# Optimization experiments

Measured on AMD Instinct MI355X. Metric: run time of the kernel, lower is better.

The kernel has to match this reference:

```python
import jax, jax.numpy as jnp
import numpy as np

B, S, D, E, F = 4, 2048, 1024, 8, 4096


def setup_inputs() -> dict:
    key = jax.random.key(0)
    k0, k1, k2, k3 = jax.random.split(key, 4)
    x = jax.random.normal(k0, (B, S, D), dtype=jnp.float32)
    wg = jax.random.normal(k1, (D, E), dtype=jnp.float32) * 0.02       # router
    w_gate = jax.random.normal(k2, (E, D, F), dtype=jnp.float32) * 0.02  # expert gate_proj
    w_down = jax.random.normal(k3, (E, F, D), dtype=jnp.float32) * 0.02  # expert down_proj
    return {"x": x, "wg": wg, "w_gate": w_gate, "w_down": w_down}


def reference(x, wg, w_gate, w_down):
    Bb, Ss, Dd = x.shape
    Ee = wg.shape[1]
    T = Bb * Ss
    C = 2 * T // Ee  # GShard top-2 capacity
    tokens = x.reshape(T, Dd)

    # ---- Top2Gate (fp32 gating) ----
    logits = tokens.astype(jnp.float32) @ wg.astype(jnp.float32)  # [T,E]
    gates = jax.nn.softmax(logits, axis=-1)
    idx1 = jnp.argmax(gates, axis=-1)                              # [T]
    mask1 = jax.nn.one_hot(idx1, Ee, dtype=jnp.int32)
    logits_no1 = jnp.where(mask1 > 0, -jnp.inf, logits)
    idx2 = jnp.argmax(logits_no1, axis=-1)
    mask2 = jax.nn.one_hot(idx2, Ee, dtype=jnp.int32)

    g1 = jnp.take_along_axis(gates, idx1[:, None], axis=-1)[:, 0]
    g2 = jnp.take_along_axis(gates, idx2[:, None], axis=-1)[:, 0]
    denom = jnp.clip(g1 + g2, 1e-9, None)
    g1, g2 = g1 / denom, g2 / denom

    # slot positions: exclusive cumsum per expert; 2nd choice offset by expert's 1st-choice count
    loc1 = jnp.cumsum(mask1, axis=0) - mask1                       # [T,E]
    loc2 = jnp.cumsum(mask2, axis=0) - mask2 + jnp.sum(mask1, axis=0, keepdims=True)
    loc1_s = jnp.sum(loc1 * mask1, axis=-1)                        # [T]
    loc2_s = jnp.sum(loc2 * mask2, axis=-1)
    keep1 = (loc1_s < C).astype(x.dtype)
    keep2 = (loc2_s < C).astype(x.dtype)

    f1 = idx1 * C + jnp.minimum(loc1_s, C - 1)                     # flat [E*C] slot ids
    f2 = idx2 * C + jnp.minimum(loc2_s, C - 1)

    # ---- dispatch (scatter, equivalent to einsum with dispatch_mask) ----
    disp = jnp.zeros((Ee * C, Dd), dtype=x.dtype)
    disp = disp.at[f1].add(tokens * keep1[:, None])
    disp = disp.at[f2].add(tokens * keep2[:, None])
    disp = disp.reshape(Ee, C, Dd)

    # ---- per-expert FFN: down_proj(gelu(gate_proj(x))) ----
    h = jax.nn.gelu(jnp.einsum('ecd,edf->ecf', disp, w_gate), approximate=False)
    eo = jnp.einsum('ecf,efd->ecd', h, w_down).reshape(Ee * C, Dd)

    # ---- combine ----
    out = (g1 * keep1)[:, None].astype(x.dtype) * eo[f1] \
        + (g2 * keep2)[:, None].astype(x.dtype) * eo[f2]
    return out.reshape(Bb, Ss, Dd)
```

## Files before the change

kernel.cpp:

```cpp
#include <hip/hip_runtime.h>
#include <hip/hip_bf16.h>
#include <math.h>

#define TT 8192
#define DDIM 1024
#define EE 8
#define FF 4096
#define CCAP 2048
#define NSLOT 16384

typedef __attribute__((ext_vector_type(4))) float f32x4;
typedef __attribute__((ext_vector_type(8))) short bf16x8;

typedef const __attribute__((address_space(1))) void CGV;
typedef __attribute__((address_space(3))) void LDSV;

__device__ __forceinline__ short f2bf(float f) {
  unsigned u = __builtin_bit_cast(unsigned, f);
  u += 0x7fffu + ((u >> 16) & 1u);
  return (short)(u >> 16);
}
__device__ __forceinline__ float bf2f(short s) {
  unsigned u = ((unsigned)(unsigned short)s) << 16;
  return __builtin_bit_cast(float, u);
}

__global__ void __launch_bounds__(256) gate_kernel(const float* __restrict__ x,
    const float* __restrict__ wg, int* __restrict__ idx1, int* __restrict__ idx2,
    float* __restrict__ g1s, float* __restrict__ g2s) {
  int lane = threadIdx.x & 63;
  int t = blockIdx.x * 4 + (threadIdx.x >> 6);
  const float* xr = x + (size_t)t * DDIM;
  float acc[8];
#pragma unroll
  for (int e = 0; e < 8; ++e) acc[e] = 0.f;
#pragma unroll
  for (int i = 0; i < 4; ++i) {
    int d = lane * 4 + i * 256;
    f32x4 xv = *(const f32x4*)(xr + d);
#pragma unroll
    for (int j = 0; j < 4; ++j) {
      const f32x4* wr = (const f32x4*)(wg + (size_t)(d + j) * 8);
      f32x4 w0 = wr[0], w1 = wr[1];
#pragma unroll
      for (int e = 0; e < 4; ++e) { acc[e] += xv[j] * w0[e]; acc[e + 4] += xv[j] * w1[e]; }
    }
  }
#pragma unroll
  for (int e = 0; e < 8; ++e) {
#pragma unroll
    for (int o = 32; o > 0; o >>= 1) acc[e] += __shfl_xor(acc[e], o, 64);
  }
  if (lane == 0) {
    int i1 = 0; float l1 = acc[0];
#pragma unroll
    for (int e = 1; e < 8; ++e) if (acc[e] > l1) { l1 = acc[e]; i1 = e; }
    int i2 = -1; float l2 = -3.0e38f;
#pragma unroll
    for (int e = 0; e < 8; ++e) if (e != i1 && acc[e] > l2) { l2 = acc[e]; i2 = e; }
    float e2 = expf(l2 - l1);
    float inv = 1.f / (1.f + e2);
    idx1[t] = i1; idx2[t] = i2;
    g1s[t] = inv; g2s[t] = e2 * inv;
  }
}

__global__ void __launch_bounds__(1024) scan_kernel(const int* __restrict__ idx1,
    const int* __restrict__ idx2, const float* __restrict__ g1s, const float* __restrict__ g2s,
    int* __restrict__ f1, int* __restrict__ f2, float* __restrict__ gg1, float* __restrict__ gg2,
    int* __restrict__ slot_token) {
  __shared__ unsigned long long slo[1024], shi[1024];
  int tid = threadIdx.x;
  for (int i = tid; i < NSLOT; i += 1024) slot_token[i] = -1;
  int t0 = tid * 8;
  int e1[8], e2[8];
#pragma unroll
  for (int i = 0; i < 8; ++i) { e1[i] = idx1[t0 + i]; e2[i] = idx2[t0 + i]; }

  unsigned long long lo = 0, hi = 0;
#pragma unroll
  for (int i = 0; i < 8; ++i) {
    int e = e1[i];
    if (e < 4) lo += 1ull << (16 * e); else hi += 1ull << (16 * (e - 4));
  }
  slo[tid] = lo; shi[tid] = hi; __syncthreads();
  for (int off = 1; off < 1024; off <<= 1) {
    unsigned long long alo = 0, ahi = 0;
    if (tid >= off) { alo = slo[tid - off]; ahi = shi[tid - off]; }
    __syncthreads();
    slo[tid] += alo; shi[tid] += ahi;
    __syncthreads();
  }
  unsigned long long exlo = slo[tid] - lo, exhi = shi[tid] - hi;
  unsigned long long tlo = slo[1023], thi = shi[1023];
  __syncthreads();
  int base1[8], tot1[8];
#pragma unroll
  for (int e = 0; e < 4; ++e) {
    base1[e]     = (int)((exlo >> (16 * e)) & 0xFFFF);
    base1[e + 4] = (int)((exhi >> (16 * e)) & 0xFFFF);
    tot1[e]      = (int)((tlo  >> (16 * e)) & 0xFFFF);
    tot1[e + 4]  = (int)((thi  >> (16 * e)) & 0xFFFF);
  }

  lo = 0; hi = 0;
#pragma unroll
  for (int i = 0; i < 8; ++i) {
    int e = e2[i];
    if (e < 4) lo += 1ull << (16 * e); else hi += 1ull << (16 * (e - 4));
  }
  slo[tid] = lo; shi[tid] = hi; __syncthreads();
  for (int off = 1; off < 1024; off <<= 1) {
    unsigned long long alo = 0, ahi = 0;
    if (tid >= off) { alo = slo[tid - off]; ahi = shi[tid - off]; }
    __syncthreads();
    slo[tid] += alo; shi[tid] += ahi;
    __syncthreads();
  }
  exlo = slo[tid] - lo; exhi = shi[tid] - hi;
  int base2[8];
#pragma unroll
  for (int e = 0; e < 4; ++e) {
    base2[e]     = (int)((exlo >> (16 * e)) & 0xFFFF);
    base2[e + 4] = (int)((exhi >> (16 * e)) & 0xFFFF);
  }

#pragma unroll
  for (int i = 0; i < 8; ++i) {
    int t = t0 + i;
    int a = e1[i];
    int p1 = base1[a]++;
    int k1 = (p1 < CCAP);
    int s1 = a * CCAP + (k1 ? p1 : CCAP - 1);
    f1[t] = s1;
    gg1[t] = k1 ? g1s[t] : 0.f;
    if (k1) slot_token[s1] = t;

    int b = e2[i];
    int p2 = base2[b] + tot1[b];
    base2[b]++;
    int k2 = (p2 < CCAP);
    int s2 = b * CCAP + (k2 ? p2 : CCAP - 1);
    f2[t] = s2;
    gg2[t] = k2 ? g2s[t] : 0.f;
    if (k2) slot_token[s2] = t;
  }
}

__global__ void __launch_bounds__(128) dispatch_kernel(const float* __restrict__ x,
    const int* __restrict__ slot_token, short* __restrict__ disp) {
  int slot = blockIdx.x;
  int tid = threadIdx.x;
  int tok = slot_token[slot];
  short* dst = disp + (size_t)slot * DDIM + tid * 8;
  bf16x8 v;
  if (tok >= 0) {
    const float* src = x + (size_t)tok * DDIM + tid * 8;
    f32x4 a = *(const f32x4*)src;
    f32x4 b = *(const f32x4*)(src + 4);
#pragma unroll
    for (int j = 0; j < 4; ++j) { v[j] = f2bf(a[j]); v[j + 4] = f2bf(b[j]); }
  } else {
#pragma unroll
    for (int j = 0; j < 8; ++j) v[j] = 0;
  }
  *(bf16x8*)dst = v;
}

__global__ void __launch_bounds__(256) tconv_kernel(const float* __restrict__ in,
    short* __restrict__ outp, int R, int Cc) {
  __shared__ float tl[32][33];
  long e = blockIdx.z;
  const float* src = in + e * (long)R * Cc;
  short* dst = outp + e * (long)R * Cc;
  int x0 = blockIdx.x * 32, y0 = blockIdx.y * 32;
  int tx = threadIdx.x, ty = threadIdx.y;
#pragma unroll
  for (int r = 0; r < 4; ++r)
    tl[ty * 4 + r][tx] = src[(long)(y0 + ty * 4 + r) * Cc + x0 + tx];
  __syncthreads();
#pragma unroll
  for (int r = 0; r < 4; ++r)
    dst[(long)(x0 + ty * 4 + r) * R + y0 + tx] = f2bf(tl[tx][ty * 4 + r]);
}

template<int KD, int LDA, int LDB, int LDC, bool GELU>
__global__ void __launch_bounds__(256) gemm_kernel(const short* __restrict__ Ag,
    const short* __restrict__ Bg, short* __restrict__ Cg,
    long aes, long bes, long ces) {
  __shared__ alignas(16) short As[128 * 32];
  __shared__ alignas(16) short Bs[128 * 32];
  int e = blockIdx.z;
  const short* A = Ag + (long)e * aes + (long)blockIdx.y * 128 * LDA;
  const short* B = Bg + (long)e * bes + (long)blockIdx.x * 128 * LDB;
  short* Cp = Cg + (long)e * ces + (long)blockIdx.y * 128 * LDC + blockIdx.x * 128;
  int tid = threadIdx.x;
  int lane = tid & 63;
  int wm = tid >> 7;
  int wn = (tid >> 6) & 1;

  f32x4 acc[4][4];
#pragma unroll
  for (int m = 0; m < 4; ++m)
#pragma unroll
    for (int n = 0; n < 4; ++n)
#pragma unroll
      for (int r = 0; r < 4; ++r) acc[m][n][r] = 0.f;

  int ga = tid;             int ra = ga >> 2, ca = (ga & 3) * 8;
  int gb = tid + 256;       int rb = gb >> 2, cb = (gb & 3) * 8;

  for (int k0 = 0; k0 < KD; k0 += 32) {
    __builtin_amdgcn_global_load_lds((CGV*)(A + (long)ra * LDA + k0 + ca),
                                     (LDSV*)(As + ga * 8), 16, 0, 0);
    __builtin_amdgcn_global_load_lds((CGV*)(A + (long)rb * LDA + k0 + cb),
                                     (LDSV*)(As + gb * 8), 16, 0, 0);
    __builtin_amdgcn_global_load_lds((CGV*)(B + (long)ra * LDB + k0 + ca),
                                     (LDSV*)(Bs + ga * 8), 16, 0, 0);
    __builtin_amdgcn_global_load_lds((CGV*)(B + (long)rb * LDB + k0 + cb),
                                     (LDSV*)(Bs + gb * 8), 16, 0, 0);
    __syncthreads();
    bf16x8 af[4], bfr[4];
    int ksel = (lane >> 4) * 8;
#pragma unroll
    for (int m = 0; m < 4; ++m)
      af[m] = *(const bf16x8*)(As + (wm * 64 + m * 16 + (lane & 15)) * 32 + ksel);
#pragma unroll
    for (int n = 0; n < 4; ++n)
      bfr[n] = *(const bf16x8*)(Bs + (wn * 64 + n * 16 + (lane & 15)) * 32 + ksel);
#pragma unroll
    for (int m = 0; m < 4; ++m)
#pragma unroll
      for (int n = 0; n < 4; ++n)
        acc[m][n] = __builtin_amdgcn_mfma_f32_16x16x32_bf16(af[m], bfr[n], acc[m][n], 0, 0, 0);
    __syncthreads();
  }

  int col0 = wn * 64 + (lane & 15);
  int row0 = wm * 64 + (lane >> 4) * 4;
#pragma unroll
  for (int m = 0; m < 4; ++m) {
#pragma unroll
    for (int r = 0; r < 4; ++r) {
      int row = row0 + m * 16 + r;
#pragma unroll
      for (int n = 0; n < 4; ++n) {
        float v = acc[m][n][r];
        if (GELU) v = 0.5f * v * (1.f + erff(v * 0.70710678118654752f));
        Cp[(long)row * LDC + col0 + n * 16] = f2bf(v);
      }
    }
  }
}

__global__ void __launch_bounds__(128) combine_kernel(const short* __restrict__ eo,
    const int* __restrict__ f1, const int* __restrict__ f2,
    const float* __restrict__ gg1, const float* __restrict__ gg2, float* __restrict__ out) {
  int t = blockIdx.x, tid = threadIdx.x;
  float a = gg1[t], b = gg2[t];
  long s1 = f1[t], s2 = f2[t];
  bf16x8 v1 = *(const bf16x8*)(eo + s1 * DDIM + tid * 8);
  bf16x8 v2 = *(const bf16x8*)(eo + s2 * DDIM + tid * 8);
  f32x4 o0, o1;
#pragma unroll
  for (int j = 0; j < 4; ++j) {
    o0[j] = a * bf2f(v1[j])     + b * bf2f(v2[j]);
    o1[j] = a * bf2f(v1[j + 4]) + b * bf2f(v2[j + 4]);
  }
  float* dst = out + (size_t)t * DDIM + tid * 8;
  *(f32x4*)dst = o0;
  *(f32x4*)(dst + 4) = o1;
}

extern "C" void kernel_launch(void* const* d_in, const int* in_sizes, int n_in,
                              void* d_out, int out_size, void* d_ws, size_t ws_size,
                              hipStream_t stream) {
  const float* x      = (const float*)d_in[0];
  const float* wg     = (const float*)d_in[1];
  const float* w_gate = (const float*)d_in[2];
  const float* w_down = (const float*)d_in[3];
  float* out = (float*)d_out;

  char* ws = (char*)d_ws;
  size_t off = 0;
  auto alloc = [&](size_t bytes) -> void* {
    void* p = ws + off;
    off += (bytes + 255) & ~(size_t)255;
    return p;
  };
  short* wbg  = (short*)alloc((size_t)EE * FF * DDIM * 2);
  short* wbd  = (short*)alloc((size_t)EE * DDIM * FF * 2);
  short* disp = (short*)alloc((size_t)NSLOT * DDIM * 2);
  short* eo   = (short*)alloc((size_t)NSLOT * DDIM * 2);
  int*   idx1 = (int*)alloc(TT * 4);
  int*   idx2 = (int*)alloc(TT * 4);
  int*   f1   = (int*)alloc(TT * 4);
  int*   f2   = (int*)alloc(TT * 4);
  float* g1s  = (float*)alloc(TT * 4);
  float* g2s  = (float*)alloc(TT * 4);
  float* gg1  = (float*)alloc(TT * 4);
  float* gg2  = (float*)alloc(TT * 4);
  int*   slot_token = (int*)alloc(NSLOT * 4);
  size_t h_full = (size_t)NSLOT * FF * 2;
  size_t h_chunk = (size_t)CCAP * FF * 2;
  bool full = (off + h_full) <= ws_size;
  short* h = (short*)(ws + off);

  tconv_kernel<<<dim3(FF / 32, DDIM / 32, EE), dim3(32, 8), 0, stream>>>(w_gate, wbg, DDIM, FF);
  tconv_kernel<<<dim3(DDIM / 32, FF / 32, EE), dim3(32, 8), 0, stream>>>(w_down, wbd, FF, DDIM);

  gate_kernel<<<TT / 4, 256, 0, stream>>>(x, wg, idx1, idx2, g1s, g2s);
  scan_kernel<<<1, 1024, 0, stream>>>(idx1, idx2, g1s, g2s, f1, f2, gg1, gg2, slot_token);
  dispatch_kernel<<<NSLOT, 128, 0, stream>>>(x, slot_token, disp);

  if (full) {
    gemm_kernel<DDIM, DDIM, DDIM, FF, true><<<dim3(FF / 128, CCAP / 128, EE), 256, 0, stream>>>(
        disp, wbg, h, (long)CCAP * DDIM, (long)FF * DDIM, (long)CCAP * FF);
    gemm_kernel<FF, FF, FF, DDIM, false><<<dim3(DDIM / 128, CCAP / 128, EE), 256, 0, stream>>>(
        h, wbd, eo, (long)CCAP * FF, (long)DDIM * FF, (long)CCAP * DDIM);
  } else {
    for (int e = 0; e < EE; ++e) {
      gemm_kernel<DDIM, DDIM, DDIM, FF, true><<<dim3(FF / 128, CCAP / 128, 1), 256, 0, stream>>>(
          disp + (long)e * CCAP * DDIM, wbg + (long)e * FF * DDIM, h, 0, 0, 0);
      gemm_kernel<FF, FF, FF, DDIM, false><<<dim3(DDIM / 128, CCAP / 128, 1), 256, 0, stream>>>(
          h, wbd + (long)e * DDIM * FF, eo + (long)e * CCAP * DDIM, 0, 0, 0);
    }
  }

  combine_kernel<<<TT, 128, 0, stream>>>(eo, f1, f2, gg1, gg2, out);
}
```

Measured before the change: 625.9 us.

## Rewrite expert GEMMs with 256x256 tiles and triple-buffered LDS pipeline

Replaces the 128x128 single-buffered bf16 MFMA GEMM with a 256x256-tile, 512-thread kernel. It triple-buffers LDS stages through async global_load_lds with explicit vmcnt/lgkmcnt waits, and double-buffers register fragments so LDS reads of the next step overlap MFMAs of the current one. It also uses a 1D grid with an XCD-aware block remap and raises MFMA wave priority. This targets latency stalls and low data reuse in the expert FFN GEMMs, which dominate runtime, at the cost of 96KB of LDS, high register pressure and fewer blocks (e.g. 256 for the down-projection GEMM).

```diff
diff --git a/kernel.cpp b/kernel.cpp
--- a/kernel.cpp
+++ b/kernel.cpp
@@ -185,69 +185,113 @@
 }
 
 template<int KD, int LDA, int LDB, int LDC, bool GELU>
-__global__ void __launch_bounds__(256) gemm_kernel(const short* __restrict__ Ag,
+__global__ void __launch_bounds__(512) gemm256(const short* __restrict__ Ag,
     const short* __restrict__ Bg, short* __restrict__ Cg,
-    long aes, long bes, long ces) {
-  __shared__ alignas(16) short As[128 * 32];
-  __shared__ alignas(16) short Bs[128 * 32];
-  int e = blockIdx.z;
-  const short* A = Ag + (long)e * aes + (long)blockIdx.y * 128 * LDA;
-  const short* B = Bg + (long)e * bes + (long)blockIdx.x * 128 * LDB;
-  short* Cp = Cg + (long)e * ces + (long)blockIdx.y * 128 * LDC + blockIdx.x * 128;
+    long aes, long bes, long ces, int nbx, int nby) {
+  constexpr int KT = KD / 32;
+  __shared__ alignas(16) short As[3][256 * 32];
+  __shared__ alignas(16) short Bs[3][256 * 32];
+
+  int bid = blockIdx.x;
+  int wid = (bid & 7) * ((int)gridDim.x >> 3) + (bid >> 3);
+  int bx = wid % nbx;
+  int rem = wid / nbx;
+  int by = rem % nby;
+  int e  = rem / nby;
+
+  const short* A = Ag + (long)e * aes + (long)by * 256 * LDA;
+  const short* B = Bg + (long)e * bes + (long)bx * 256 * LDB;
+  short* Cp = Cg + (long)e * ces + (long)by * 256 * LDC + bx * 256;
+
   int tid = threadIdx.x;
-  int lane = tid & 63;
-  int wm = tid >> 7;
-  int wn = (tid >> 6) & 1;
-
-  f32x4 acc[4][4];
-#pragma unroll
-  for (int m = 0; m < 4; ++m)
+  int l = tid & 63;
+  int w = tid >> 6;
+  int wm = w >> 2, wn = w & 3;
+
+  f32x4 acc[8][4];
+#pragma unroll
+  for (int m = 0; m < 8; ++m)
 #pragma unroll
     for (int n = 0; n < 4; ++n)
 #pragma unroll
       for (int r = 0; r < 4; ++r) acc[m][n][r] = 0.f;
 
-  int ga = tid;             int ra = ga >> 2, ca = (ga & 3) * 8;
-  int gb = tid + 256;       int rb = gb >> 2, cb = (gb & 3) * 8;
-
-  for (int k0 = 0; k0 < KD; k0 += 32) {
-    __builtin_amdgcn_global_load_lds((CGV*)(A + (long)ra * LDA + k0 + ca),
-                                     (LDSV*)(As + ga * 8), 16, 0, 0);
-    __builtin_amdgcn_global_load_lds((CGV*)(A + (long)rb * LDA + k0 + cb),
-                                     (LDSV*)(As + gb * 8), 16, 0, 0);
-    __builtin_amdgcn_global_load_lds((CGV*)(B + (long)ra * LDB + k0 + ca),
-                                     (LDSV*)(Bs + ga * 8), 16, 0, 0);
-    __builtin_amdgcn_global_load_lds((CGV*)(B + (long)rb * LDB + k0 + cb),
-                                     (LDSV*)(Bs + gb * 8), 16, 0, 0);
-    __syncthreads();
-    bf16x8 af[4], bfr[4];
-    int ksel = (lane >> 4) * 8;
-#pragma unroll
-    for (int m = 0; m < 4; ++m)
-      af[m] = *(const bf16x8*)(As + (wm * 64 + m * 16 + (lane & 15)) * 32 + ksel);
-#pragma unroll
-    for (int n = 0; n < 4; ++n)
-      bfr[n] = *(const bf16x8*)(Bs + (wn * 64 + n * 16 + (lane & 15)) * 32 + ksel);
-#pragma unroll
-    for (int m = 0; m < 4; ++m)
+  auto STAGE = [&](int slot, int k0) {
+#pragma unroll
+    for (int c = 0; c < 2; ++c) {
+      int g = c * 512 + tid;
+      int r = g >> 2, col = (g & 3) * 8;
+      __builtin_amdgcn_global_load_lds((CGV*)(A + (long)r * LDA + k0 + col),
+                                       (LDSV*)(&As[slot][g * 8]), 16, 0, 0);
+      __builtin_amdgcn_global_load_lds((CGV*)(B + (long)r * LDB + k0 + col),
+                                       (LDSV*)(&Bs[slot][g * 8]), 16, 0, 0);
+    }
+  };
+
+  int abase = (wm * 128 + (l & 15)) * 32 + (l >> 4) * 8;
+  int bbase = (wn * 64 + (l & 15)) * 32 + (l >> 4) * 8;
+  auto DSREAD = [&](bf16x8* fa, bf16x8* fb, int slot) {
+    const short* a = &As[slot][abase];
+    const short* b = &Bs[slot][bbase];
+#pragma unroll
+    for (int m = 0; m < 8; ++m) fa[m] = *(const bf16x8*)(a + m * 512);
+#pragma unroll
+    for (int n = 0; n < 4; ++n) fb[n] = *(const bf16x8*)(b + n * 512);
+  };
+  auto MFMA = [&](bf16x8* fa, bf16x8* fb) {
+    __builtin_amdgcn_s_setprio(1);
+#pragma unroll
+    for (int m = 0; m < 8; ++m)
 #pragma unroll
       for (int n = 0; n < 4; ++n)
-        acc[m][n] = __builtin_amdgcn_mfma_f32_16x16x32_bf16(af[m], bfr[n], acc[m][n], 0, 0, 0);
-    __syncthreads();
-  }
-
-  int col0 = wn * 64 + (lane & 15);
-  int row0 = wm * 64 + (lane >> 4) * 4;
-#pragma unroll
-  for (int m = 0; m < 4; ++m) {
+        acc[m][n] = __builtin_amdgcn_mfma_f32_16x16x32_bf16(fa[m], fb[n], acc[m][n], 0, 0, 0);
+    __builtin_amdgcn_s_setprio(0);
+  };
+
+  bf16x8 fA0[8], fB0[4], fA1[8], fB1[4];
+
+  STAGE(0, 0); STAGE(1, 32); STAGE(2, 64);
+  asm volatile("s_waitcnt vmcnt(4)" ::: "memory");
+  __builtin_amdgcn_sched_barrier(0);
+  __builtin_amdgcn_s_barrier();
+  __builtin_amdgcn_sched_barrier(0);
+  DSREAD(fA0, fB0, 0);
+  asm volatile("s_waitcnt lgkmcnt(0)" ::: "memory");
+  __builtin_amdgcn_sched_barrier(0);
+  __builtin_amdgcn_s_barrier();
+  __builtin_amdgcn_sched_barrier(0);
+
+  int sl = 0;
+  auto ITER = [&](int t, bf16x8* fcA, bf16x8* fcB, bf16x8* fnA, bf16x8* fnB) {
+    if (t + 3 < KT) STAGE(sl, (t + 3) * 32);
+    int rs = (sl == 2) ? 0 : sl + 1;
+    if (t + 1 < KT) DSREAD(fnA, fnB, rs);
+    MFMA(fcA, fcB);
+    asm volatile("s_waitcnt lgkmcnt(0)" ::: "memory");
+    __builtin_amdgcn_sched_barrier(0);
+    if (t + 3 < KT) { asm volatile("s_waitcnt vmcnt(4)" ::: "memory"); }
+    else            { asm volatile("s_waitcnt vmcnt(0)" ::: "memory"); }
+    __builtin_amdgcn_sched_barrier(0);
+    __builtin_amdgcn_s_barrier();
+    __builtin_amdgcn_sched_barrier(0);
+    sl = (sl == 2) ? 0 : sl + 1;
+  };
+
+  for (int t = 0; t < KT; t += 2) {
+    ITER(t,     fA0, fB0, fA1, fB1);
+    ITER(t + 1, fA1, fB1, fA0, fB0);
+  }
+
+#pragma unroll
+  for (int m = 0; m < 8; ++m) {
+    int gr0 = wm * 128 + m * 16 + (l >> 4) * 4;
 #pragma unroll
     for (int r = 0; r < 4; ++r) {
-      int row = row0 + m * 16 + r;
 #pragma unroll
       for (int n = 0; n < 4; ++n) {
         float v = acc[m][n][r];
         if (GELU) v = 0.5f * v * (1.f + erff(v * 0.70710678118654752f));
-        Cp[(long)row * LDC + col0 + n * 16] = f2bf(v);
+        Cp[(long)(gr0 + r) * LDC + wn * 64 + n * 16 + (l & 15)] = f2bf(v);
       }
     }
   }
@@ -302,7 +346,6 @@
   float* gg2  = (float*)alloc(TT * 4);
   int*   slot_token = (int*)alloc(NSLOT * 4);
   size_t h_full = (size_t)NSLOT * FF * 2;
-  size_t h_chunk = (size_t)CCAP * FF * 2;
   bool full = (off + h_full) <= ws_size;
   short* h = (short*)(ws + off);
 
@@ -314,16 +357,16 @@
   dispatch_kernel<<<NSLOT, 128, 0, stream>>>(x, slot_token, disp);
 
   if (full) {
-    gemm_kernel<DDIM, DDIM, DDIM, FF, true><<<dim3(FF / 128, CCAP / 128, EE), 256, 0, stream>>>(
-        disp, wbg, h, (long)CCAP * DDIM, (long)FF * DDIM, (long)CCAP * FF);
-    gemm_kernel<FF, FF, FF, DDIM, false><<<dim3(DDIM / 128, CCAP / 128, EE), 256, 0, stream>>>(
-        h, wbd, eo, (long)CCAP * FF, (long)DDIM * FF, (long)CCAP * DDIM);
+    gemm256<DDIM, DDIM, DDIM, FF, true><<<(FF / 256) * (CCAP / 256) * EE, 512, 0, stream>>>(
+        disp, wbg, h, (long)CCAP * DDIM, (long)FF * DDIM, (long)CCAP * FF, FF / 256, CCAP / 256);
+    gemm256<FF, FF, FF, DDIM, false><<<(DDIM / 256) * (CCAP / 256) * EE, 512, 0, stream>>>(
+        h, wbd, eo, (long)CCAP * FF, (long)DDIM * FF, (long)CCAP * DDIM, DDIM / 256, CCAP / 256);
   } else {
     for (int e = 0; e < EE; ++e) {
-      gemm_kernel<DDIM, DDIM, DDIM, FF, true><<<dim3(FF / 128, CCAP / 128, 1), 256, 0, stream>>>(
-          disp + (long)e * CCAP * DDIM, wbg + (long)e * FF * DDIM, h, 0, 0, 0);
-      gemm_kernel<FF, FF, FF, DDIM, false><<<dim3(DDIM / 128, CCAP / 128, 1), 256, 0, stream>>>(
-          h, wbd + (long)e * DDIM * FF, eo + (long)e * CCAP * DDIM, 0, 0, 0);
+      gemm256<DDIM, DDIM, DDIM, FF, true><<<(FF / 256) * (CCAP / 256), 512, 0, stream>>>(
+          disp + (long)e * CCAP * DDIM, wbg + (long)e * FF * DDIM, h, 0, 0, 0, FF / 256, CCAP / 256);
+      gemm256<FF, FF, FF, DDIM, false><<<(DDIM / 256) * (CCAP / 256), 512, 0, stream>>>(
+          h, wbd + (long)e * DDIM * FF, eo + (long)e * CCAP * DDIM, 0, 0, 0, DDIM / 256, CCAP / 256);
     }
   }
 
```

New measurement: 649.7 us. 1.04x slower.
